# Optimization experiments

Measured on AMD Instinct MI355X. Metric: run time of the kernel, lower is better.

## Reference

```python
import jax, jax.numpy as jnp
import numpy as np

B, S, D, H = 8, 2048, 512, 8
NEG = -1e9


def setup_inputs() -> dict:
    key = jax.random.key(0)
    ks = jax.random.split(key, 12)
    inp = {
        "v": jax.random.normal(ks[0], (B, S, D), jnp.float32),
        "k": jax.random.normal(ks[1], (B, S, D), jnp.float32),
        "q": jax.random.normal(ks[2], (B, S, D), jnp.float32),
    }
    # pad_mask: 1.0 where key position is padding ([B,1,1,S]); random valid lengths
    lens = jax.random.randint(ks[3], (B,), S // 2, S + 1)
    inp["pad_mask"] = (jnp.arange(S)[None, :] >= lens[:, None]).astype(jnp.float32)[:, None, None, :]
    # head_mask: causal look-ahead mask, 1.0 above diagonal ([1,1,S,S])
    inp["head_mask"] = jnp.triu(jnp.ones((S, S), jnp.float32), k=1)[None, None]
    # Dense layer params (Keras Dense: y = x @ W + b)
    sc = 1.0 / np.sqrt(D)
    inp["Wq"] = jax.random.normal(ks[4], (D, D), jnp.float32) * sc
    inp["bq"] = jnp.zeros((D,), jnp.float32)
    inp["Wk"] = jax.random.normal(ks[5], (D, D), jnp.float32) * sc
    inp["bk"] = jnp.zeros((D,), jnp.float32)
    inp["Wv"] = jax.random.normal(ks[6], (D, D), jnp.float32) * sc
    inp["bv"] = jnp.zeros((D,), jnp.float32)
    inp["Wo"] = jax.random.normal(ks[7], (D, D), jnp.float32) * sc
    inp["bo"] = jnp.zeros((D,), jnp.float32)
    inp["num_heads"] = H
    return inp


def reference(v, k, q, pad_mask, head_mask, Wq, bq, Wk, bk, Wv, bv, Wo, bo, num_heads):
    b, s, d = q.shape
    depth = d // num_heads

    def split_heads(x):  # [b,s,d] -> [b,h,s,depth]
        return x.reshape(b, -1, num_heads, depth).transpose(0, 2, 1, 3)

    qh = split_heads(q @ Wq + bq)
    kh = split_heads(k @ Wk + bk)
    vh = split_heads(v @ Wv + bv)

    scale = 1.0 / jnp.sqrt(jnp.asarray(depth, qh.dtype))
    scores = jnp.einsum("bhqd,bhkd->bhqk", qh, kh) * scale
    scores = scores + pad_mask * NEG + head_mask * NEG
    attn = jax.nn.softmax(scores, axis=-1)
    ctx = jnp.einsum("bhqk,bhkd->bhqd", attn, vh)
    concat = ctx.transpose(0, 2, 1, 3).reshape(b, -1, d)
    return concat @ Wo + bo
```

## Files before the change

kernel.cpp:

```cpp
#include <hip/hip_runtime.h>

#define B_ 8
#define S_ 2048
#define D_ 512
#define H_ 8
#define HD_ 64

typedef __attribute__((ext_vector_type(8))) short short8;
typedef __attribute__((ext_vector_type(4))) short short4v;
typedef __attribute__((ext_vector_type(4))) float f32x4;
typedef __attribute__((ext_vector_type(16))) float f32x16;
typedef __attribute__((ext_vector_type(8))) __bf16 bf16x8;
typedef __attribute__((ext_vector_type(4))) unsigned uint4v;

__device__ __forceinline__ short f2bf(float f) {
    union { float f; unsigned u; } x; x.f = f;
    unsigned r = x.u + 0x7fffu + ((x.u >> 16) & 1u);
    return (short)(r >> 16);
}

__device__ __forceinline__ unsigned cvtpk(float a, float b) {
    unsigned r;
    asm("v_cvt_pk_bf16_f32 %0, %1, %2" : "=v"(r) : "v"(a), "v"(b));
    return r;
}

__device__ __forceinline__ f32x4 mfma16(short8 a, short8 b, f32x4 c) {
    return __builtin_amdgcn_mfma_f32_16x16x32_bf16(
        __builtin_bit_cast(bf16x8, a), __builtin_bit_cast(bf16x8, b), c, 0, 0, 0);
}

__device__ __forceinline__ f32x16 mfma32(short8 a, short8 b, f32x16 c) {
    return __builtin_amdgcn_mfma_f32_32x32x16_bf16(
        __builtin_bit_cast(bf16x8, a), __builtin_bit_cast(bf16x8, b), c, 0, 0, 0);
}

__device__ __forceinline__ f32x16 zero16() {
    f32x16 z;
    #pragma unroll
    for (int i = 0; i < 16; ++i) z[i] = 0.f;
    return z;
}

__global__ __launch_bounds__(256) void prep_wt(
    const float* __restrict__ W0, const float* __restrict__ W1,
    const float* __restrict__ W2, const float* __restrict__ W3,
    short* __restrict__ T0, short* __restrict__ T1,
    short* __restrict__ T2, short* __restrict__ T3)
{
    const float* W = (blockIdx.z == 0) ? W0 : (blockIdx.z == 1) ? W1 : (blockIdx.z == 2) ? W2 : W3;
    short* T = (blockIdx.z == 0) ? T0 : (blockIdx.z == 1) ? T1 : (blockIdx.z == 2) ? T2 : T3;
    __shared__ float t_s[64][65];
    const int tid = threadIdx.x;
    const int k0 = blockIdx.x * 64, n0 = blockIdx.y * 64;
    const int col = tid & 63, rg = tid >> 6;
    #pragma unroll
    for (int j = 0; j < 16; ++j) {
        const int row = rg * 16 + j;
        t_s[row][col] = W[(size_t)(k0 + row) * D_ + n0 + col];
    }
    __syncthreads();
    #pragma unroll
    for (int j = 0; j < 16; ++j) {
        const int nn = rg * 16 + j;
        T[(size_t)(n0 + nn) * D_ + k0 + col] = f2bf(t_s[col][nn]);
    }
}

__global__ __launch_bounds__(512) void qkv_gemm(
    const float* __restrict__ q_in, const float* __restrict__ k_in, const float* __restrict__ v_in,
    const short* __restrict__ wtq, const short* __restrict__ wtk, const short* __restrict__ wtv,
    const float* __restrict__ bq, const float* __restrict__ bk, const float* __restrict__ bv,
    short* __restrict__ qh, short* __restrict__ kh, short* __restrict__ vtb, float qscale)
{
    const int id = blockIdx.x;
    const int xcd = id & 7;
    const int slot = id >> 3;
    const int n0 = (slot & 3) * 128;
    const int pidx = xcd * 48 + (slot >> 2);
    const int z = pidx >> 7;
    const int m0 = (pidx & 127) * 128;

    const float* Ain = (z == 0) ? q_in : (z == 1) ? k_in : v_in;
    const short* Wt  = (z == 0) ? wtq  : (z == 1) ? wtk  : wtv;
    const float* bias = (z == 0) ? bq : (z == 1) ? bk : bv;
    short* Cout = (z == 0) ? qh : (z == 1) ? kh : vtb;
    const float osc = (z == 0) ? qscale : 1.0f;
    const int N = D_, K = D_;

    __shared__ __align__(16) short a_s[2][128 * 72];
    __shared__ __align__(16) short bt_s[2][128 * 72];

    const int tid = threadIdx.x;
    const int lane = tid & 63, wave = tid >> 6;
    const int wr = wave >> 2, wc = wave & 3;
    const int lr = lane & 15, lg = lane >> 4;

    const int srow = tid >> 3, sch = (tid & 7) * 8;

    f32x4 acc[4][2] = {};

    f32x4 fa[4];
    short8 bs[2];
    {
        const f32x4* ap0 = (const f32x4*)(Ain + (size_t)(m0 + srow) * K + sch);
        fa[0] = ap0[0]; fa[1] = ap0[1];
        const f32x4* ap1 = (const f32x4*)(Ain + (size_t)(m0 + srow + 64) * K + sch);
        fa[2] = ap1[0]; fa[3] = ap1[1];
        bs[0] = *(const short8*)(Wt + (size_t)(n0 + srow) * K + sch);
        bs[1] = *(const short8*)(Wt + (size_t)(n0 + srow + 64) * K + sch);
    }

    int cur = 0;
    for (int k0 = 0; k0 < K; k0 += 64) {
        {
            const uint4v u0 = { cvtpk(fa[0][0], fa[0][1]), cvtpk(fa[0][2], fa[0][3]),
                                cvtpk(fa[1][0], fa[1][1]), cvtpk(fa[1][2], fa[1][3]) };
            *(short8*)&a_s[cur][srow * 72 + sch] = __builtin_bit_cast(short8, u0);
            const uint4v u1 = { cvtpk(fa[2][0], fa[2][1]), cvtpk(fa[2][2], fa[2][3]),
                                cvtpk(fa[3][0], fa[3][1]), cvtpk(fa[3][2], fa[3][3]) };
            *(short8*)&a_s[cur][(srow + 64) * 72 + sch] = __builtin_bit_cast(short8, u1);
            *(short8*)&bt_s[cur][srow * 72 + sch] = bs[0];
            *(short8*)&bt_s[cur][(srow + 64) * 72 + sch] = bs[1];
        }
        __syncthreads();
        if (k0 + 64 < K) {
            const f32x4* ap0 = (const f32x4*)(Ain + (size_t)(m0 + srow) * K + k0 + 64 + sch);
            fa[0] = ap0[0]; fa[1] = ap0[1];
            const f32x4* ap1 = (const f32x4*)(Ain + (size_t)(m0 + srow + 64) * K + k0 + 64 + sch);
            fa[2] = ap1[0]; fa[3] = ap1[1];
            bs[0] = *(const short8*)(Wt + (size_t)(n0 + srow) * K + k0 + 64 + sch);
            bs[1] = *(const short8*)(Wt + (size_t)(n0 + srow + 64) * K + k0 + 64 + sch);
        }

        #pragma unroll
        for (int kc = 0; kc < 2; ++kc) {
            short8 af[4], bf[2];
            #pragma unroll
            for (int m = 0; m < 4; ++m)
                af[m] = *(const short8*)&a_s[cur][(wr * 64 + m * 16 + lr) * 72 + kc * 32 + lg * 8];
            #pragma unroll
            for (int n = 0; n < 2; ++n)
                bf[n] = *(const short8*)&bt_s[cur][(wc * 32 + n * 16 + lr) * 72 + kc * 32 + lg * 8];
            __builtin_amdgcn_s_setprio(1);
            #pragma unroll
            for (int m = 0; m < 4; ++m)
                #pragma unroll
                for (int n = 0; n < 2; ++n)
                    acc[m][n] = mfma16(af[m], bf[n], acc[m][n]);
            __builtin_amdgcn_s_setprio(0);
        }
        cur ^= 1;
    }

    float bvv[2];
    #pragma unroll
    for (int n = 0; n < 2; ++n) bvv[n] = bias[n0 + wc * 32 + n * 16 + lr];

    if (z == 2) {
        #pragma unroll
        for (int m = 0; m < 4; ++m) {
            const int row0 = m0 + wr * 64 + m * 16 + lg * 4;
            const int bb = row0 >> 11, s0 = row0 & (S_ - 1);
            #pragma unroll
            for (int n = 0; n < 2; ++n) {
                const int col = n0 + wc * 32 + n * 16 + lr;
                uint2 wv;
                wv.x = cvtpk(acc[m][n][0] + bvv[n], acc[m][n][1] + bvv[n]);
                wv.y = cvtpk(acc[m][n][2] + bvv[n], acc[m][n][3] + bvv[n]);
                *(uint2*)(Cout + ((size_t)col * B_ + bb) * S_ + s0) = wv;
            }
        }
    } else {
        #pragma unroll
        for (int m = 0; m < 4; ++m)
            #pragma unroll
            for (int i = 0; i < 4; ++i) {
                const size_t row = m0 + wr * 64 + m * 16 + lg * 4 + i;
                #pragma unroll
                for (int n = 0; n < 2; ++n) {
                    const int col = n0 + wc * 32 + n * 16 + lr;
                    Cout[row * N + col] = f2bf((acc[m][n][i] + bvv[n]) * osc);
                }
            }
    }
}

__global__ __launch_bounds__(512) void out_gemm(
    const short* __restrict__ Ain, const short* __restrict__ Wt,
    const float* __restrict__ bias, float* __restrict__ Cout)
{
    const int id = blockIdx.x;
    const int xcd = id & 7;
    const int slot = id >> 3;
    const int n0 = (slot & 3) * 128;
    const int m0 = (xcd * 16 + (slot >> 2)) * 128;
    const int N = D_, K = D_;

    __shared__ __align__(16) short a_s[2][128 * 72];
    __shared__ __align__(16) short bt_s[2][128 * 72];

    const int tid = threadIdx.x;
    const int lane = tid & 63, wave = tid >> 6;
    const int wr = wave >> 2, wc = wave & 3;
    const int lr = lane & 15, lg = lane >> 4;
    const int srow = tid >> 3, sch = (tid & 7) * 8;

    f32x4 acc[4][2] = {};

    short8 as[2], bs[2];
    {
        as[0] = *(const short8*)(Ain + (size_t)(m0 + srow) * K + sch);
        as[1] = *(const short8*)(Ain + (size_t)(m0 + srow + 64) * K + sch);
        bs[0] = *(const short8*)(Wt + (size_t)(n0 + srow) * K + sch);
        bs[1] = *(const short8*)(Wt + (size_t)(n0 + srow + 64) * K + sch);
    }

    int cur = 0;
    for (int k0 = 0; k0 < K; k0 += 64) {
        *(short8*)&a_s[cur][srow * 72 + sch] = as[0];
        *(short8*)&a_s[cur][(srow + 64) * 72 + sch] = as[1];
        *(short8*)&bt_s[cur][srow * 72 + sch] = bs[0];
        *(short8*)&bt_s[cur][(srow + 64) * 72 + sch] = bs[1];
        __syncthreads();
        if (k0 + 64 < K) {
            as[0] = *(const short8*)(Ain + (size_t)(m0 + srow) * K + k0 + 64 + sch);
            as[1] = *(const short8*)(Ain + (size_t)(m0 + srow + 64) * K + k0 + 64 + sch);
            bs[0] = *(const short8*)(Wt + (size_t)(n0 + srow) * K + k0 + 64 + sch);
            bs[1] = *(const short8*)(Wt + (size_t)(n0 + srow + 64) * K + k0 + 64 + sch);
        }

        #pragma unroll
        for (int kc = 0; kc < 2; ++kc) {
            short8 af[4], bf[2];
            #pragma unroll
            for (int m = 0; m < 4; ++m)
                af[m] = *(const short8*)&a_s[cur][(wr * 64 + m * 16 + lr) * 72 + kc * 32 + lg * 8];
            #pragma unroll
            for (int n = 0; n < 2; ++n)
                bf[n] = *(const short8*)&bt_s[cur][(wc * 32 + n * 16 + lr) * 72 + kc * 32 + lg * 8];
            __builtin_amdgcn_s_setprio(1);
            #pragma unroll
            for (int m = 0; m < 4; ++m)
                #pragma unroll
                for (int n = 0; n < 2; ++n)
                    acc[m][n] = mfma16(af[m], bf[n], acc[m][n]);
            __builtin_amdgcn_s_setprio(0);
        }
        cur ^= 1;
    }

    float bvv[2];
    #pragma unroll
    for (int n = 0; n < 2; ++n) bvv[n] = bias[n0 + wc * 32 + n * 16 + lr];
    #pragma unroll
    for (int m = 0; m < 4; ++m)
        #pragma unroll
        for (int i = 0; i < 4; ++i) {
            const size_t row = m0 + wr * 64 + m * 16 + lg * 4 + i;
            #pragma unroll
            for (int n = 0; n < 2; ++n)
                Cout[row * N + n0 + wc * 32 + n * 16 + lr] = acc[m][n][i] + bvv[n];
        }
}

__global__ __launch_bounds__(128, 3) void attn_k(
    const short* __restrict__ qh, const short* __restrict__ kh,
    const short* __restrict__ vt, const float* __restrict__ pad_mask,
    short* __restrict__ ctx)
{
    const int tid = threadIdx.x;
    const int lane = tid & 63, w = tid >> 6;
    const int l31 = lane & 31, hi = lane >> 5;
    const int id = blockIdx.x;
    const int h = id & 7;
    const int b = (id >> 3) & 7;
    const int pair = id >> 6;
    const int NT = S_ / 64;

    __shared__ __align__(16) short k_s[2][64 * 72];
    __shared__ __align__(16) short vt_s[2][64 * 68];
    __shared__ float red_s[2];

    const float* pb = pad_mask + (size_t)b * S_;
    {
        const f32x4* pv4 = (const f32x4*)pb;
        float psum = 0.f;
        #pragma unroll
        for (int j = 0; j < 4; ++j) {
            const f32x4 a = pv4[tid * 4 + j];
            psum += a[0] + a[1] + a[2] + a[3];
        }
        for (int off = 1; off < 64; off <<= 1) psum += __shfl_xor(psum, off);
        if (lane == 0) red_s[w] = psum;
    }
    __syncthreads();
    const int len = S_ - (int)(red_s[0] + red_s[1] + 0.5f);

    const int srow = tid >> 1, sc0 = (tid & 1) * 32;
    const short* kbase = kh + ((size_t)b * S_ + srow) * D_ + h * HD_ + sc0;
    const short* vbase = vt + ((size_t)(h * HD_ + srow) * B_ + b) * S_ + sc0;

    int cur = 0;
    for (int half = 0; half < 2; ++half) {
        const int qt = half ? (NT - 1 - pair) : pair;
        const int q0 = qt * 64;
        const int kt_end = min(qt, (len - 1) >> 6);

        const int qrow = q0 + 2 * l31 + w;
        const short* qptr = qh + ((size_t)b * S_ + qrow) * D_ + h * HD_ + hi * 8;
        short8 qf[4];
        #pragma unroll
        for (int dd = 0; dd < 4; ++dd) qf[dd] = *(const short8*)(qptr + dd * 16);

        f32x16 accA = zero16(), accB = zero16();
        float m_r = -1e30f, l_r = 0.f;
        const int kmax = min(qrow, len - 1);

        short8 kv[4], vv[4];
        #pragma unroll
        for (int p = 0; p < 4; ++p) {
            kv[p] = ((const short8*)kbase)[p];
            vv[p] = ((const short8*)vbase)[p];
        }

        for (int kt = 0; kt <= kt_end; ++kt) {
            #pragma unroll
            for (int p = 0; p < 4; ++p)
                *(short8*)&k_s[cur][srow * 72 + sc0 + p * 8] = kv[p];
            #pragma unroll
            for (int p = 0; p < 4; ++p) {
                *(short4v*)&vt_s[cur][srow * 68 + sc0 + p * 8]     = __builtin_shufflevector(vv[p], vv[p], 0, 1, 2, 3);
                *(short4v*)&vt_s[cur][srow * 68 + sc0 + p * 8 + 4] = __builtin_shufflevector(vv[p], vv[p], 4, 5, 6, 7);
            }
            __syncthreads();
            if (kt < kt_end) {
                const short* kp = kbase + (size_t)(kt + 1) * 64 * D_;
                const short* vp = vbase + (kt + 1) * 64;
                #pragma unroll
                for (int p = 0; p < 4; ++p) {
                    kv[p] = ((const short8*)kp)[p];
                    vv[p] = ((const short8*)vp)[p];
                }
            }

            f32x16 scA = zero16(), scB = zero16();
            __builtin_amdgcn_s_setprio(1);
            #pragma unroll
            for (int dd = 0; dd < 4; ++dd) {
                const short8 kfA = *(const short8*)&k_s[cur][l31 * 72 + dd * 16 + hi * 8];
                const short8 kfB = *(const short8*)&k_s[cur][(32 + l31) * 72 + dd * 16 + hi * 8];
                scA = mfma32(kfA, qf[dd], scA);
                scB = mfma32(kfB, qf[dd], scB);
            }
            __builtin_amdgcn_s_setprio(0);

            const bool needmask = (kt == qt) || (kt * 64 + 63 >= len);
            if (needmask) {
                #pragma unroll
                for (int reg = 0; reg < 16; ++reg) {
                    const int koff = kt * 64 + (reg & 3) + 8 * (reg >> 2) + 4 * hi;
                    if (koff > kmax)      scA[reg] = -1e30f;
                    if (koff + 32 > kmax) scB[reg] = -1e30f;
                }
            }

            float m8[8], m4[4];
            #pragma unroll
            for (int i = 0; i < 8; ++i) m8[i] = fmaxf(fmaxf(scA[i], scA[i + 8]), fmaxf(scB[i], scB[i + 8]));
            #pragma unroll
            for (int i = 0; i < 4; ++i) m4[i] = fmaxf(m8[i], m8[i + 4]);
            float mt = fmaxf(fmaxf(m4[0], m4[1]), fmaxf(m4[2], m4[3]));
            mt = fmaxf(mt, __shfl_xor(mt, 32));
            const bool nogrow = __all(mt <= m_r);
            const float mn = nogrow ? m_r : fmaxf(m_r, mt);

            #pragma unroll
            for (int i = 0; i < 16; ++i) {
                scA[i] = __builtin_amdgcn_exp2f(scA[i] - mn);
                scB[i] = __builtin_amdgcn_exp2f(scB[i] - mn);
            }
            float s8[8], s4[4];
            #pragma unroll
            for (int i = 0; i < 8; ++i) s8[i] = (scA[i] + scA[i + 8]) + (scB[i] + scB[i + 8]);
            #pragma unroll
            for (int i = 0; i < 4; ++i) s4[i] = s8[i] + s8[i + 4];
            float rs = (s4[0] + s4[1]) + (s4[2] + s4[3]);
            rs += __shfl_xor(rs, 32);

            if (nogrow) {
                l_r += rs;
            } else {
                const float fac = __builtin_amdgcn_exp2f(m_r - mn);
                l_r = l_r * fac + rs;
                m_r = mn;
                #pragma unroll
                for (int reg = 0; reg < 16; ++reg) { accA[reg] *= fac; accB[reg] *= fac; }
            }

            unsigned pw[4][4];
            #pragma unroll
            for (int kk = 0; kk < 4; ++kk) {
                const int g = kk & 1;
                unsigned w0, w1, w2, w3;
                if (kk < 2) {
                    w0 = cvtpk(scA[8 * g + 0], scA[8 * g + 1]);
                    w1 = cvtpk(scA[8 * g + 2], scA[8 * g + 3]);
                    w2 = cvtpk(scA[8 * g + 4], scA[8 * g + 5]);
                    w3 = cvtpk(scA[8 * g + 6], scA[8 * g + 7]);
                } else {
                    w0 = cvtpk(scB[8 * g + 0], scB[8 * g + 1]);
                    w1 = cvtpk(scB[8 * g + 2], scB[8 * g + 3]);
                    w2 = cvtpk(scB[8 * g + 4], scB[8 * g + 5]);
                    w3 = cvtpk(scB[8 * g + 6], scB[8 * g + 7]);
                }
                asm("v_permlane32_swap_b32 %0, %1" : "+v"(w0), "+v"(w2));
                asm("v_permlane32_swap_b32 %0, %1" : "+v"(w1), "+v"(w3));
                pw[kk][0] = w0; pw[kk][1] = w1; pw[kk][2] = w2; pw[kk][3] = w3;
            }

            __builtin_amdgcn_s_setprio(1);
            #pragma unroll
            for (int kk = 0; kk < 4; ++kk) {
                const uint4v u = { pw[kk][0], pw[kk][1], pw[kk][2], pw[kk][3] };
                const short8 pf = __builtin_bit_cast(short8, u);
                const short4v a0 = *(const short4v*)&vt_s[cur][l31 * 68 + kk * 16 + 8 * hi];
                const short4v a1 = *(const short4v*)&vt_s[cur][l31 * 68 + kk * 16 + 8 * hi + 4];
                const short8 afA = __builtin_shufflevector(a0, a1, 0, 1, 2, 3, 4, 5, 6, 7);
                accA = mfma32(afA, pf, accA);
                const short4v b0 = *(const short4v*)&vt_s[cur][(32 + l31) * 68 + kk * 16 + 8 * hi];
                const short4v b1 = *(const short4v*)&vt_s[cur][(32 + l31) * 68 + kk * 16 + 8 * hi + 4];
                const short8 afB = __builtin_shufflevector(b0, b1, 0, 1, 2, 3, 4, 5, 6, 7);
                accB = mfma32(afB, pf, accB);
            }
            __builtin_amdgcn_s_setprio(0);
            cur ^= 1;
        }

        const float li = __builtin_amdgcn_rcpf(l_r);
        short* cp = ctx + ((size_t)b * S_ + qrow) * D_ + h * HD_ + 4 * hi;
        #pragma unroll
        for (int g = 0; g < 4; ++g) {
            uint2 wa;
            wa.x = cvtpk(accA[4 * g + 0] * li, accA[4 * g + 1] * li);
            wa.y = cvtpk(accA[4 * g + 2] * li, accA[4 * g + 3] * li);
            *(uint2*)(cp + 8 * g) = wa;
            uint2 wb;
            wb.x = cvtpk(accB[4 * g + 0] * li, accB[4 * g + 1] * li);
            wb.y = cvtpk(accB[4 * g + 2] * li, accB[4 * g + 3] * li);
            *(uint2*)(cp + 32 + 8 * g) = wb;
        }
    }
}

extern "C" void kernel_launch(void* const* d_in, const int* in_sizes, int n_in,
                              void* d_out, int out_size, void* d_ws, size_t ws_size,
                              hipStream_t stream)
{
    const float* v_in = (const float*)d_in[0];
    const float* k_in = (const float*)d_in[1];
    const float* q_in = (const float*)d_in[2];
    const float* pad  = (const float*)d_in[3];
    const float* Wq = (const float*)d_in[5];  const float* bq = (const float*)d_in[6];
    const float* Wk = (const float*)d_in[7];  const float* bk = (const float*)d_in[8];
    const float* Wv = (const float*)d_in[9];  const float* bv = (const float*)d_in[10];
    const float* Wo = (const float*)d_in[11]; const float* bo = (const float*)d_in[12];

    const size_t elems = (size_t)B_ * S_ * D_;
    const size_t welems = (size_t)D_ * D_;
    short* qh  = (short*)d_ws;
    short* kh  = qh + elems;
    short* vtb = kh + elems;
    short* ctx = vtb + elems;
    short* wtq = ctx + elems;
    short* wtk = wtq + welems;
    short* wtv = wtk + welems;
    short* wto = wtv + welems;

    prep_wt<<<dim3(D_ / 64, D_ / 64, 4), dim3(256), 0, stream>>>(Wq, Wk, Wv, Wo, wtq, wtk, wtv, wto);

    const float qscale = 0.125f * 1.4426950408889634f;
    qkv_gemm<<<dim3(1536), dim3(512), 0, stream>>>(
        q_in, k_in, v_in, wtq, wtk, wtv, bq, bk, bv, qh, kh, vtb, qscale);

    attn_k<<<dim3(1024), dim3(128), 0, stream>>>(qh, kh, vtb, pad, ctx);

    out_gemm<<<dim3(512), dim3(512), 0, stream>>>(ctx, wto, bo, (float*)d_out);
}
```

Measured before the change: 135.6 us.

## Split attention KV loop across two waves with 32-row query tiles

The attention kernel now processes 32-query tiles (grid doubled to 2048 blocks). The two waves in each block take alternating 32-key tiles independently, each with its own LDS buffer, so the per-iteration block barrier goes away. At the end the two partial softmax states and accumulators are merged through shared memory. Occupancy hint raised from 3 to 4 blocks. This trades halved MFMA work per wave step and an extra cross-wave merge for finer load balance and no intra-loop syncs.

```diff
diff --git a/kernel.cpp b/kernel.cpp
--- a/kernel.cpp
+++ b/kernel.cpp
@@ -95,7 +95,6 @@
     const int lane = tid & 63, wave = tid >> 6;
     const int wr = wave >> 2, wc = wave & 3;
     const int lr = lane & 15, lg = lane >> 4;
-
     const int srow = tid >> 3, sch = (tid & 7) * 8;
 
     f32x4 acc[4][2] = {};
@@ -264,7 +263,7 @@
         }
 }
 
-__global__ __launch_bounds__(128, 3) void attn_k(
+__global__ __launch_bounds__(128, 4) void attn_k(
     const short* __restrict__ qh, const short* __restrict__ kh,
     const short* __restrict__ vt, const float* __restrict__ pad_mask,
     short* __restrict__ ctx)
@@ -275,11 +274,10 @@
     const int id = blockIdx.x;
     const int h = id & 7;
     const int b = (id >> 3) & 7;
-    const int pair = id >> 6;
-    const int NT = S_ / 64;
-
-    __shared__ __align__(16) short k_s[2][64 * 72];
-    __shared__ __align__(16) short vt_s[2][64 * 68];
+    const int p = id >> 6;
+
+    __shared__ __align__(16) short k_s[2][32 * 68];
+    __shared__ __align__(16) short vs_s[2][64 * 36];
     __shared__ float red_s[2];
 
     const float* pb = pad_mask + (size_t)b * S_;
@@ -297,17 +295,21 @@
     __syncthreads();
     const int len = S_ - (int)(red_s[0] + red_s[1] + 0.5f);
 
-    const int srow = tid >> 1, sc0 = (tid & 1) * 32;
-    const short* kbase = kh + ((size_t)b * S_ + srow) * D_ + h * HD_ + sc0;
-    const short* vbase = vt + ((size_t)(h * HD_ + srow) * B_ + b) * S_ + sc0;
-
-    int cur = 0;
+    const int ksr = lane >> 1, ksc = (lane & 1) * 32;
+    const short* kbase = kh + ((size_t)b * S_ + ksr) * D_ + h * HD_ + ksc;
+    const short* vbase = vt + ((size_t)(h * HD_ + lane) * B_ + b) * S_;
+
+    float* accx = (float*)&k_s[0][0];
+    float* mx = (float*)&vs_s[0][0];
+    float* lx = mx + 128;
+
     for (int half = 0; half < 2; ++half) {
-        const int qt = half ? (NT - 1 - pair) : pair;
-        const int q0 = qt * 64;
-        const int kt_end = min(qt, (len - 1) >> 6);
-
-        const int qrow = q0 + 2 * l31 + w;
+        const int qt = half ? (63 - p) : p;
+        const int q0 = qt * 32;
+        const int kt_end = min(qt, (len - 1) >> 5);
+        const int qrow = q0 + l31;
+        const int kmax = min(qrow, len - 1);
+
         const short* qptr = qh + ((size_t)b * S_ + qrow) * D_ + h * HD_ + hi * 8;
         short8 qf[4];
         #pragma unroll
@@ -315,59 +317,52 @@
 
         f32x16 accA = zero16(), accB = zero16();
         float m_r = -1e30f, l_r = 0.f;
-        const int kmax = min(qrow, len - 1);
-
+
+        int kt = w;
         short8 kv[4], vv[4];
-        #pragma unroll
-        for (int p = 0; p < 4; ++p) {
-            kv[p] = ((const short8*)kbase)[p];
-            vv[p] = ((const short8*)vbase)[p];
-        }
-
-        for (int kt = 0; kt <= kt_end; ++kt) {
-            #pragma unroll
-            for (int p = 0; p < 4; ++p)
-                *(short8*)&k_s[cur][srow * 72 + sc0 + p * 8] = kv[p];
-            #pragma unroll
-            for (int p = 0; p < 4; ++p) {
-                *(short4v*)&vt_s[cur][srow * 68 + sc0 + p * 8]     = __builtin_shufflevector(vv[p], vv[p], 0, 1, 2, 3);
-                *(short4v*)&vt_s[cur][srow * 68 + sc0 + p * 8 + 4] = __builtin_shufflevector(vv[p], vv[p], 4, 5, 6, 7);
-            }
-            __syncthreads();
-            if (kt < kt_end) {
-                const short* kp = kbase + (size_t)(kt + 1) * 64 * D_;
-                const short* vp = vbase + (kt + 1) * 64;
-                #pragma unroll
-                for (int p = 0; p < 4; ++p) {
-                    kv[p] = ((const short8*)kp)[p];
-                    vv[p] = ((const short8*)vp)[p];
+        if (kt <= kt_end) {
+            #pragma unroll
+            for (int pp = 0; pp < 4; ++pp) {
+                kv[pp] = *(const short8*)(kbase + (size_t)kt * 32 * D_ + pp * 8);
+                vv[pp] = *(const short8*)(vbase + kt * 32 + pp * 8);
+            }
+        }
+
+        for (; kt <= kt_end; kt += 2) {
+            #pragma unroll
+            for (int pp = 0; pp < 4; ++pp)
+                *(short8*)&k_s[w][ksr * 68 + ksc + pp * 8] = kv[pp];
+            #pragma unroll
+            for (int pp = 0; pp < 4; ++pp)
+                *(short8*)&vs_s[w][lane * 36 + pp * 8] = vv[pp];
+            if (kt + 2 <= kt_end) {
+                #pragma unroll
+                for (int pp = 0; pp < 4; ++pp) {
+                    kv[pp] = *(const short8*)(kbase + (size_t)(kt + 2) * 32 * D_ + pp * 8);
+                    vv[pp] = *(const short8*)(vbase + (kt + 2) * 32 + pp * 8);
                 }
             }
 
-            f32x16 scA = zero16(), scB = zero16();
+            f32x16 sc = zero16();
             __builtin_amdgcn_s_setprio(1);
             #pragma unroll
             for (int dd = 0; dd < 4; ++dd) {
-                const short8 kfA = *(const short8*)&k_s[cur][l31 * 72 + dd * 16 + hi * 8];
-                const short8 kfB = *(const short8*)&k_s[cur][(32 + l31) * 72 + dd * 16 + hi * 8];
-                scA = mfma32(kfA, qf[dd], scA);
-                scB = mfma32(kfB, qf[dd], scB);
+                const short8 kf = *(const short8*)&k_s[w][l31 * 68 + dd * 16 + hi * 8];
+                sc = mfma32(kf, qf[dd], sc);
             }
             __builtin_amdgcn_s_setprio(0);
 
-            const bool needmask = (kt == qt) || (kt * 64 + 63 >= len);
-            if (needmask) {
+            if (kt == qt || kt * 32 + 31 >= len) {
                 #pragma unroll
                 for (int reg = 0; reg < 16; ++reg) {
-                    const int koff = kt * 64 + (reg & 3) + 8 * (reg >> 2) + 4 * hi;
-                    if (koff > kmax)      scA[reg] = -1e30f;
-                    if (koff + 32 > kmax) scB[reg] = -1e30f;
+                    const int koff = kt * 32 + (reg & 3) + 8 * (reg >> 2) + 4 * hi;
+                    if (koff > kmax) sc[reg] = -1e30f;
                 }
             }
 
             float m8[8], m4[4];
             #pragma unroll
-            for (int i = 0; i < 8; ++i) m8[i] = fmaxf(fmaxf(scA[i], scA[i + 8]), fmaxf(scB[i], scB[i + 8]));
+            for (int i = 0; i < 8; ++i) m8[i] = fmaxf(sc[i], sc[i + 8]);
             #pragma unroll
             for (int i = 0; i < 4; ++i) m4[i] = fmaxf(m8[i], m8[i + 4]);
             float mt = fmaxf(fmaxf(m4[0], m4[1]), fmaxf(m4[2], m4[3]));
@@ -376,13 +371,10 @@
             const float mn = nogrow ? m_r : fmaxf(m_r, mt);
 
             #pragma unroll
-            for (int i = 0; i < 16; ++i) {
-                scA[i] = __builtin_amdgcn_exp2f(scA[i] - mn);
-                scB[i] = __builtin_amdgcn_exp2f(scB[i] - mn);
-            }
+            for (int i = 0; i < 16; ++i) sc[i] = __builtin_amdgcn_exp2f(sc[i] - mn);
             float s8[8], s4[4];
             #pragma unroll
-            for (int i = 0; i < 8; ++i) s8[i] = (scA[i] + scA[i + 8]) + (scB[i] + scB[i + 8]);
+            for (int i = 0; i < 8; ++i) s8[i] = sc[i] + sc[i + 8];
             #pragma unroll
             for (int i = 0; i < 4; ++i) s4[i] = s8[i] + s8[i + 4];
             float rs = (s4[0] + s4[1]) + (s4[2] + s4[3]);
@@ -398,22 +390,13 @@
                 for (int reg = 0; reg < 16; ++reg) { accA[reg] *= fac; accB[reg] *= fac; }
             }
 
-            unsigned pw[4][4];
-            #pragma unroll
-            for (int kk = 0; kk < 4; ++kk) {
-                const int g = kk & 1;
-                unsigned w0, w1, w2, w3;
-                if (kk < 2) {
-                    w0 = cvtpk(scA[8 * g + 0], scA[8 * g + 1]);
-                    w1 = cvtpk(scA[8 * g + 2], scA[8 * g + 3]);
-                    w2 = cvtpk(scA[8 * g + 4], scA[8 * g + 5]);
-                    w3 = cvtpk(scA[8 * g + 6], scA[8 * g + 7]);
-                } else {
-                    w0 = cvtpk(scB[8 * g + 0], scB[8 * g + 1]);
-                    w1 = cvtpk(scB[8 * g + 2], scB[8 * g + 3]);
-                    w2 = cvtpk(scB[8 * g + 4], scB[8 * g + 5]);
-                    w3 = cvtpk(scB[8 * g + 6], scB[8 * g + 7]);
-                }
+            unsigned pw[2][4];
+            #pragma unroll
+            for (int kk = 0; kk < 2; ++kk) {
+                unsigned w0 = cvtpk(sc[8 * kk + 0], sc[8 * kk + 1]);
+                unsigned w1 = cvtpk(sc[8 * kk + 2], sc[8 * kk + 3]);
+                unsigned w2 = cvtpk(sc[8 * kk + 4], sc[8 * kk + 5]);
+                unsigned w3 = cvtpk(sc[8 * kk + 6], sc[8 * kk + 7]);
                 asm("v_permlane32_swap_b32 %0, %1" : "+v"(w0), "+v"(w2));
                 asm("v_permlane32_swap_b32 %0, %1" : "+v"(w1), "+v"(w3));
                 pw[kk][0] = w0; pw[kk][1] = w1; pw[kk][2] = w2; pw[kk][3] = w3;
@@ -421,35 +404,58 @@
 
             __builtin_amdgcn_s_setprio(1);
             #pragma unroll
-            for (int kk = 0; kk < 4; ++kk) {
+            for (int kk = 0; kk < 2; ++kk) {
                 const uint4v u = { pw[kk][0], pw[kk][1], pw[kk][2], pw[kk][3] };
                 const short8 pf = __builtin_bit_cast(short8, u);
-                const short4v a0 = *(const short4v*)&vt_s[cur][l31 * 68 + kk * 16 + 8 * hi];
-                const short4v a1 = *(const short4v*)&vt_s[cur][l31 * 68 + kk * 16 + 8 * hi + 4];
+                const short4v a0 = *(const short4v*)&vs_s[w][l31 * 36 + kk * 16 + 8 * hi];
+                const short4v a1 = *(const short4v*)&vs_s[w][l31 * 36 + kk * 16 + 8 * hi + 4];
                 const short8 afA = __builtin_shufflevector(a0, a1, 0, 1, 2, 3, 4, 5, 6, 7);
                 accA = mfma32(afA, pf, accA);
-                const short4v b0 = *(const short4v*)&vt_s[cur][(32 + l31) * 68 + kk * 16 + 8 * hi];
-                const short4v b1 = *(const short4v*)&vt_s[cur][(32 + l31) * 68 + kk * 16 + 8 * hi + 4];
+                const short4v b0 = *(const short4v*)&vs_s[w][(32 + l31) * 36 + kk * 16 + 8 * hi];
+                const short4v b1 = *(const short4v*)&vs_s[w][(32 + l31) * 36 + kk * 16 + 8 * hi + 4];
                 const short8 afB = __builtin_shufflevector(b0, b1, 0, 1, 2, 3, 4, 5, 6, 7);
                 accB = mfma32(afB, pf, accB);
             }
             __builtin_amdgcn_s_setprio(0);
-            cur ^= 1;
-        }
-
-        const float li = __builtin_amdgcn_rcpf(l_r);
-        short* cp = ctx + ((size_t)b * S_ + qrow) * D_ + h * HD_ + 4 * hi;
-        #pragma unroll
-        for (int g = 0; g < 4; ++g) {
-            uint2 wa;
-            wa.x = cvtpk(accA[4 * g + 0] * li, accA[4 * g + 1] * li);
-            wa.y = cvtpk(accA[4 * g + 2] * li, accA[4 * g + 3] * li);
-            *(uint2*)(cp + 8 * g) = wa;
-            uint2 wb;
-            wb.x = cvtpk(accB[4 * g + 0] * li, accB[4 * g + 1] * li);
-            wb.y = cvtpk(accB[4 * g + 2] * li, accB[4 * g + 3] * li);
-            *(uint2*)(cp + 32 + 8 * g) = wb;
-        }
+        }
+
+        __syncthreads();
+        mx[w * 64 + lane] = m_r;
+        lx[w * 64 + lane] = l_r;
+        __syncthreads();
+        const float mo = mx[(w ^ 1) * 64 + lane];
+        const float lo = lx[(w ^ 1) * 64 + lane];
+        const float mj = fmaxf(m_r, mo);
+        const float facS = __builtin_amdgcn_exp2f(m_r - mj);
+        const float facO = __builtin_amdgcn_exp2f(mo - mj);
+        const float l_tot = l_r * facS + lo * facO;
+        if (w == 1) {
+            #pragma unroll
+            for (int i = 0; i < 16; ++i) accx[i * 64 + lane] = accA[i] * facS;
+            #pragma unroll
+            for (int i = 0; i < 16; ++i) accx[(16 + i) * 64 + lane] = accB[i] * facS;
+        }
+        __syncthreads();
+        if (w == 0) {
+            const float li = __builtin_amdgcn_rcpf(l_tot);
+            short* cp = ctx + ((size_t)b * S_ + qrow) * D_ + h * HD_ + 4 * hi;
+            #pragma unroll
+            for (int g = 0; g < 4; ++g) {
+                float o0 = (accA[4 * g + 0] * facS + accx[(4 * g + 0) * 64 + lane]) * li;
+                float o1 = (accA[4 * g + 1] * facS + accx[(4 * g + 1) * 64 + lane]) * li;
+                float o2 = (accA[4 * g + 2] * facS + accx[(4 * g + 2) * 64 + lane]) * li;
+                float o3 = (accA[4 * g + 3] * facS + accx[(4 * g + 3) * 64 + lane]) * li;
+                uint2 wa; wa.x = cvtpk(o0, o1); wa.y = cvtpk(o2, o3);
+                *(uint2*)(cp + 8 * g) = wa;
+                float p0 = (accB[4 * g + 0] * facS + accx[(16 + 4 * g + 0) * 64 + lane]) * li;
+                float p1 = (accB[4 * g + 1] * facS + accx[(16 + 4 * g + 1) * 64 + lane]) * li;
+                float p2 = (accB[4 * g + 2] * facS + accx[(16 + 4 * g + 2) * 64 + lane]) * li;
+                float p3 = (accB[4 * g + 3] * facS + accx[(16 + 4 * g + 3) * 64 + lane]) * li;
+                uint2 wb; wb.x = cvtpk(p0, p1); wb.y = cvtpk(p2, p3);
+                *(uint2*)(cp + 32 + 8 * g) = wb;
+            }
+        }
+        __syncthreads();
     }
 }
 
@@ -483,7 +489,7 @@
     qkv_gemm<<<dim3(1536), dim3(512), 0, stream>>>(
         q_in, k_in, v_in, wtq, wtk, wtv, bq, bk, bv, qh, kh, vtb, qscale);
 
-    attn_k<<<dim3(1024), dim3(128), 0, stream>>>(qh, kh, vtb, pad, ctx);
+    attn_k<<<dim3(2048), dim3(128), 0, stream>>>(qh, kh, vtb, pad, ctx);
 
     out_gemm<<<dim3(512), dim3(512), 0, stream>>>(ctx, wto, bo, (float*)d_out);
 }
```

New measurement: 195.3 us. +44.1%, slower.

## Make attention waves independent with per-wave K/V tiles and no block barriers

Applied to the files above, without the earlier changes.

Restructures the attention kernel so each of the two waves in a block owns a 32-row query tile (paired causally as p and 63-p) and stages its own 64-key K/V tile in a private LDS slot. This removes all __syncthreads from the key loop and the shared pad-mask reduction, and the grid is doubled to 2048 blocks. Each wave now loads a full K/V tile by itself, so global and LDS traffic per query row doubles, the single LDS buffer per wave loses double buffering, and launch bounds drop to 2 blocks per SIMD.

```diff
diff --git a/kernel.cpp b/kernel.cpp
--- a/kernel.cpp
+++ b/kernel.cpp
@@ -95,7 +95,6 @@
     const int lane = tid & 63, wave = tid >> 6;
     const int wr = wave >> 2, wc = wave & 3;
     const int lr = lane & 15, lg = lane >> 4;
-
     const int srow = tid >> 3, sch = (tid & 7) * 8;
 
     f32x4 acc[4][2] = {};
@@ -264,7 +263,7 @@
         }
 }
 
-__global__ __launch_bounds__(128, 3) void attn_k(
+__global__ __launch_bounds__(128, 2) void attn_k(
     const short* __restrict__ qh, const short* __restrict__ kh,
     const short* __restrict__ vt, const float* __restrict__ pad_mask,
     short* __restrict__ ctx)
@@ -275,181 +274,170 @@
     const int id = blockIdx.x;
     const int h = id & 7;
     const int b = (id >> 3) & 7;
-    const int pair = id >> 6;
-    const int NT = S_ / 64;
+    const int p = id >> 6;
 
     __shared__ __align__(16) short k_s[2][64 * 72];
     __shared__ __align__(16) short vt_s[2][64 * 68];
-    __shared__ float red_s[2];
-
-    const float* pb = pad_mask + (size_t)b * S_;
+
+    float psum = 0.f;
     {
-        const f32x4* pv4 = (const f32x4*)pb;
-        float psum = 0.f;
-        #pragma unroll
-        for (int j = 0; j < 4; ++j) {
-            const f32x4 a = pv4[tid * 4 + j];
-            psum += a[0] + a[1] + a[2] + a[3];
-        }
+        const f32x4* pv4 = (const f32x4*)(pad_mask + (size_t)b * S_);
+        #pragma unroll
+        for (int j = 0; j < 8; ++j) {
+            const f32x4 a = pv4[lane * 8 + j];
+            psum += (a[0] + a[1]) + (a[2] + a[3]);
+        }
+        #pragma unroll
         for (int off = 1; off < 64; off <<= 1) psum += __shfl_xor(psum, off);
-        if (lane == 0) red_s[w] = psum;
-    }
-    __syncthreads();
-    const int len = S_ - (int)(red_s[0] + red_s[1] + 0.5f);
-
-    const int srow = tid >> 1, sc0 = (tid & 1) * 32;
-    const short* kbase = kh + ((size_t)b * S_ + srow) * D_ + h * HD_ + sc0;
-    const short* vbase = vt + ((size_t)(h * HD_ + srow) * B_ + b) * S_ + sc0;
-
-    int cur = 0;
-    for (int half = 0; half < 2; ++half) {
-        const int qt = half ? (NT - 1 - pair) : pair;
-        const int q0 = qt * 64;
-        const int kt_end = min(qt, (len - 1) >> 6);
-
-        const int qrow = q0 + 2 * l31 + w;
-        const short* qptr = qh + ((size_t)b * S_ + qrow) * D_ + h * HD_ + hi * 8;
-        short8 qf[4];
-        #pragma unroll
-        for (int dd = 0; dd < 4; ++dd) qf[dd] = *(const short8*)(qptr + dd * 16);
-
-        f32x16 accA = zero16(), accB = zero16();
-        float m_r = -1e30f, l_r = 0.f;
-        const int kmax = min(qrow, len - 1);
-
-        short8 kv[4], vv[4];
-        #pragma unroll
-        for (int p = 0; p < 4; ++p) {
-            kv[p] = ((const short8*)kbase)[p];
-            vv[p] = ((const short8*)vbase)[p];
-        }
-
-        for (int kt = 0; kt <= kt_end; ++kt) {
-            #pragma unroll
-            for (int p = 0; p < 4; ++p)
-                *(short8*)&k_s[cur][srow * 72 + sc0 + p * 8] = kv[p];
-            #pragma unroll
-            for (int p = 0; p < 4; ++p) {
-                *(short4v*)&vt_s[cur][srow * 68 + sc0 + p * 8]     = __builtin_shufflevector(vv[p], vv[p], 0, 1, 2, 3);
-                *(short4v*)&vt_s[cur][srow * 68 + sc0 + p * 8 + 4] = __builtin_shufflevector(vv[p], vv[p], 4, 5, 6, 7);
+    }
+    const int len = S_ - (int)(psum + 0.5f);
+    const int lenT = (len - 1) >> 6;
+
+    const int qt = w ? (63 - p) : p;
+    const int q0 = qt * 32;
+    const int diag = qt >> 1;
+    const int kt_end = min(diag, lenT);
+    const int qrow = q0 + l31;
+    const int kmax = min(qrow, len - 1);
+
+    const short* qptr = qh + ((size_t)b * S_ + qrow) * D_ + h * HD_ + hi * 8;
+    short8 qf[4];
+    #pragma unroll
+    for (int dd = 0; dd < 4; ++dd) qf[dd] = *(const short8*)(qptr + dd * 16);
+
+    f32x16 accA = zero16(), accB = zero16();
+    float m_r = -1e30f, l_r = 0.f;
+
+    const short* kbase = kh + ((size_t)b * S_ + lane) * D_ + h * HD_;
+    const short* vbase = vt + ((size_t)(h * HD_ + lane) * B_ + b) * S_;
+
+    short8 kv[8], vv[8];
+    #pragma unroll
+    for (int pp = 0; pp < 8; ++pp) {
+        kv[pp] = *(const short8*)(kbase + pp * 8);
+        vv[pp] = *(const short8*)(vbase + pp * 8);
+    }
+
+    for (int kt = 0; kt <= kt_end; ++kt) {
+        #pragma unroll
+        for (int pp = 0; pp < 8; ++pp)
+            *(short8*)&k_s[w][lane * 72 + pp * 8] = kv[pp];
+        #pragma unroll
+        for (int pp = 0; pp < 8; ++pp)
+            *(short8*)&vt_s[w][lane * 68 + pp * 8] = vv[pp];
+        if (kt < kt_end) {
+            const short* kp = kbase + (size_t)(kt + 1) * 64 * D_;
+            const short* vp = vbase + (kt + 1) * 64;
+            #pragma unroll
+            for (int pp = 0; pp < 8; ++pp) {
+                kv[pp] = *(const short8*)(kp + pp * 8);
+                vv[pp] = *(const short8*)(vp + pp * 8);
             }
-            __syncthreads();
-            if (kt < kt_end) {
-                const short* kp = kbase + (size_t)(kt + 1) * 64 * D_;
-                const short* vp = vbase + (kt + 1) * 64;
-                #pragma unroll
-                for (int p = 0; p < 4; ++p) {
-                    kv[p] = ((const short8*)kp)[p];
-                    vv[p] = ((const short8*)vp)[p];
-                }
+        }
+
+        f32x16 scA = zero16(), scB = zero16();
+        __builtin_amdgcn_s_setprio(1);
+        #pragma unroll
+        for (int dd = 0; dd < 4; ++dd) {
+            const short8 kfA = *(const short8*)&k_s[w][l31 * 72 + dd * 16 + hi * 8];
+            const short8 kfB = *(const short8*)&k_s[w][(32 + l31) * 72 + dd * 16 + hi * 8];
+            scA = mfma32(kfA, qf[dd], scA);
+            scB = mfma32(kfB, qf[dd], scB);
+        }
+        __builtin_amdgcn_s_setprio(0);
+
+        if (kt == diag || kt * 64 + 63 >= len) {
+            #pragma unroll
+            for (int reg = 0; reg < 16; ++reg) {
+                const int koff = kt * 64 + (reg & 3) + 8 * (reg >> 2) + 4 * hi;
+                if (koff > kmax)      scA[reg] = -1e30f;
+                if (koff + 32 > kmax) scB[reg] = -1e30f;
             }
-
-            f32x16 scA = zero16(), scB = zero16();
-            __builtin_amdgcn_s_setprio(1);
-            #pragma unroll
-            for (int dd = 0; dd < 4; ++dd) {
-                const short8 kfA = *(const short8*)&k_s[cur][l31 * 72 + dd * 16 + hi * 8];
-                const short8 kfB = *(const short8*)&k_s[cur][(32 + l31) * 72 + dd * 16 + hi * 8];
-                scA = mfma32(kfA, qf[dd], scA);
-                scB = mfma32(kfB, qf[dd], scB);
+        }
+
+        float m8[8], m4[4];
+        #pragma unroll
+        for (int i = 0; i < 8; ++i) m8[i] = fmaxf(fmaxf(scA[i], scA[i + 8]), fmaxf(scB[i], scB[i + 8]));
+        #pragma unroll
+        for (int i = 0; i < 4; ++i) m4[i] = fmaxf(m8[i], m8[i + 4]);
+        float mt = fmaxf(fmaxf(m4[0], m4[1]), fmaxf(m4[2], m4[3]));
+        mt = fmaxf(mt, __shfl_xor(mt, 32));
+        const bool nogrow = __all(mt <= m_r);
+        const float mn = nogrow ? m_r : fmaxf(m_r, mt);
+
+        #pragma unroll
+        for (int i = 0; i < 16; ++i) {
+            scA[i] = __builtin_amdgcn_exp2f(scA[i] - mn);
+            scB[i] = __builtin_amdgcn_exp2f(scB[i] - mn);
+        }
+        float s8[8], s4[4];
+        #pragma unroll
+        for (int i = 0; i < 8; ++i) s8[i] = (scA[i] + scA[i + 8]) + (scB[i] + scB[i + 8]);
+        #pragma unroll
+        for (int i = 0; i < 4; ++i) s4[i] = s8[i] + s8[i + 4];
+        float rs = (s4[0] + s4[1]) + (s4[2] + s4[3]);
+        rs += __shfl_xor(rs, 32);
+
+        if (nogrow) {
+            l_r += rs;
+        } else {
+            const float fac = __builtin_amdgcn_exp2f(m_r - mn);
+            l_r = l_r * fac + rs;
+            m_r = mn;
+            #pragma unroll
+            for (int reg = 0; reg < 16; ++reg) { accA[reg] *= fac; accB[reg] *= fac; }
+        }
+
+        unsigned pw[4][4];
+        #pragma unroll
+        for (int kk = 0; kk < 4; ++kk) {
+            const int g = kk & 1;
+            unsigned w0, w1, w2, w3;
+            if (kk < 2) {
+                w0 = cvtpk(scA[8 * g + 0], scA[8 * g + 1]);
+                w1 = cvtpk(scA[8 * g + 2], scA[8 * g + 3]);
+                w2 = cvtpk(scA[8 * g + 4], scA[8 * g + 5]);
+                w3 = cvtpk(scA[8 * g + 6], scA[8 * g + 7]);
+            } else {
+                w0 = cvtpk(scB[8 * g + 0], scB[8 * g + 1]);
+                w1 = cvtpk(scB[8 * g + 2], scB[8 * g + 3]);
+                w2 = cvtpk(scB[8 * g + 4], scB[8 * g + 5]);
+                w3 = cvtpk(scB[8 * g + 6], scB[8 * g + 7]);
             }
-            __builtin_amdgcn_s_setprio(0);
-
-            const bool needmask = (kt == qt) || (kt * 64 + 63 >= len);
-            if (needmask) {
-                #pragma unroll
-                for (int reg = 0; reg < 16; ++reg) {
-                    const int koff = kt * 64 + (reg & 3) + 8 * (reg >> 2) + 4 * hi;
-                    if (koff > kmax)      scA[reg] = -1e30f;
-                    if (koff + 32 > kmax) scB[reg] = -1e30f;
-                }
-            }
-
-            float m8[8], m4[4];
-            #pragma unroll
-            for (int i = 0; i < 8; ++i) m8[i] = fmaxf(fmaxf(scA[i], scA[i + 8]), fmaxf(scB[i], scB[i + 8]));
-            #pragma unroll
-            for (int i = 0; i < 4; ++i) m4[i] = fmaxf(m8[i], m8[i + 4]);
-            float mt = fmaxf(fmaxf(m4[0], m4[1]), fmaxf(m4[2], m4[3]));
-            mt = fmaxf(mt, __shfl_xor(mt, 32));
-            const bool nogrow = __all(mt <= m_r);
-            const float mn = nogrow ? m_r : fmaxf(m_r, mt);
-
-            #pragma unroll
-            for (int i = 0; i < 16; ++i) {
-                scA[i] = __builtin_amdgcn_exp2f(scA[i] - mn);
-                scB[i] = __builtin_amdgcn_exp2f(scB[i] - mn);
-            }
-            float s8[8], s4[4];
-            #pragma unroll
-            for (int i = 0; i < 8; ++i) s8[i] = (scA[i] + scA[i + 8]) + (scB[i] + scB[i + 8]);
-            #pragma unroll
-            for (int i = 0; i < 4; ++i) s4[i] = s8[i] + s8[i + 4];
-            float rs = (s4[0] + s4[1]) + (s4[2] + s4[3]);
-            rs += __shfl_xor(rs, 32);
-
-            if (nogrow) {
-                l_r += rs;
-            } else {
-                const float fac = __builtin_amdgcn_exp2f(m_r - mn);
-                l_r = l_r * fac + rs;
-                m_r = mn;
-                #pragma unroll
-                for (int reg = 0; reg < 16; ++reg) { accA[reg] *= fac; accB[reg] *= fac; }
-            }
-
-            unsigned pw[4][4];
-            #pragma unroll
-            for (int kk = 0; kk < 4; ++kk) {
-                const int g = kk & 1;
-                unsigned w0, w1, w2, w3;
-                if (kk < 2) {
-                    w0 = cvtpk(scA[8 * g + 0], scA[8 * g + 1]);
-                    w1 = cvtpk(scA[8 * g + 2], scA[8 * g + 3]);
-                    w2 = cvtpk(scA[8 * g + 4], scA[8 * g + 5]);
-                    w3 = cvtpk(scA[8 * g + 6], scA[8 * g + 7]);
-                } else {
-                    w0 = cvtpk(scB[8 * g + 0], scB[8 * g + 1]);
-                    w1 = cvtpk(scB[8 * g + 2], scB[8 * g + 3]);
-                    w2 = cvtpk(scB[8 * g + 4], scB[8 * g + 5]);
-                    w3 = cvtpk(scB[8 * g + 6], scB[8 * g + 7]);
-                }
-                asm("v_permlane32_swap_b32 %0, %1" : "+v"(w0), "+v"(w2));
-                asm("v_permlane32_swap_b32 %0, %1" : "+v"(w1), "+v"(w3));
-                pw[kk][0] = w0; pw[kk][1] = w1; pw[kk][2] = w2; pw[kk][3] = w3;
-            }
-
-            __builtin_amdgcn_s_setprio(1);
-            #pragma unroll
-            for (int kk = 0; kk < 4; ++kk) {
-                const uint4v u = { pw[kk][0], pw[kk][1], pw[kk][2], pw[kk][3] };
-                const short8 pf = __builtin_bit_cast(short8, u);
-                const short4v a0 = *(const short4v*)&vt_s[cur][l31 * 68 + kk * 16 + 8 * hi];
-                const short4v a1 = *(const short4v*)&vt_s[cur][l31 * 68 + kk * 16 + 8 * hi + 4];
-                const short8 afA = __builtin_shufflevector(a0, a1, 0, 1, 2, 3, 4, 5, 6, 7);
-                accA = mfma32(afA, pf, accA);
-                const short4v b0 = *(const short4v*)&vt_s[cur][(32 + l31) * 68 + kk * 16 + 8 * hi];
-                const short4v b1 = *(const short4v*)&vt_s[cur][(32 + l31) * 68 + kk * 16 + 8 * hi + 4];
-                const short8 afB = __builtin_shufflevector(b0, b1, 0, 1, 2, 3, 4, 5, 6, 7);
-                accB = mfma32(afB, pf, accB);
-            }
-            __builtin_amdgcn_s_setprio(0);
-            cur ^= 1;
-        }
-
-        const float li = __builtin_amdgcn_rcpf(l_r);
-        short* cp = ctx + ((size_t)b * S_ + qrow) * D_ + h * HD_ + 4 * hi;
-        #pragma unroll
-        for (int g = 0; g < 4; ++g) {
-            uint2 wa;
-            wa.x = cvtpk(accA[4 * g + 0] * li, accA[4 * g + 1] * li);
-            wa.y = cvtpk(accA[4 * g + 2] * li, accA[4 * g + 3] * li);
-            *(uint2*)(cp + 8 * g) = wa;
-            uint2 wb;
-            wb.x = cvtpk(accB[4 * g + 0] * li, accB[4 * g + 1] * li);
-            wb.y = cvtpk(accB[4 * g + 2] * li, accB[4 * g + 3] * li);
-            *(uint2*)(cp + 32 + 8 * g) = wb;
-        }
+            asm("v_permlane32_swap_b32 %0, %1" : "+v"(w0), "+v"(w2));
+            asm("v_permlane32_swap_b32 %0, %1" : "+v"(w1), "+v"(w3));
+            pw[kk][0] = w0; pw[kk][1] = w1; pw[kk][2] = w2; pw[kk][3] = w3;
+        }
+
+        __builtin_amdgcn_s_setprio(1);
+        #pragma unroll
+        for (int kk = 0; kk < 4; ++kk) {
+            const uint4v u = { pw[kk][0], pw[kk][1], pw[kk][2], pw[kk][3] };
+            const short8 pf = __builtin_bit_cast(short8, u);
+            const short4v a0 = *(const short4v*)&vt_s[w][l31 * 68 + kk * 16 + 8 * hi];
+            const short4v a1 = *(const short4v*)&vt_s[w][l31 * 68 + kk * 16 + 8 * hi + 4];
+            const short8 afA = __builtin_shufflevector(a0, a1, 0, 1, 2, 3, 4, 5, 6, 7);
+            accA = mfma32(afA, pf, accA);
+            const short4v b0 = *(const short4v*)&vt_s[w][(32 + l31) * 68 + kk * 16 + 8 * hi];
+            const short4v b1 = *(const short4v*)&vt_s[w][(32 + l31) * 68 + kk * 16 + 8 * hi + 4];
+            const short8 afB = __builtin_shufflevector(b0, b1, 0, 1, 2, 3, 4, 5, 6, 7);
+            accB = mfma32(afB, pf, accB);
+        }
+        __builtin_amdgcn_s_setprio(0);
+    }
+
+    const float li = __builtin_amdgcn_rcpf(l_r);
+    short* cp = ctx + ((size_t)b * S_ + qrow) * D_ + h * HD_ + 4 * hi;
+    #pragma unroll
+    for (int g = 0; g < 4; ++g) {
+        uint2 wa;
+        wa.x = cvtpk(accA[4 * g + 0] * li, accA[4 * g + 1] * li);
+        wa.y = cvtpk(accA[4 * g + 2] * li, accA[4 * g + 3] * li);
+        *(uint2*)(cp + 8 * g) = wa;
+        uint2 wb;
+        wb.x = cvtpk(accB[4 * g + 0] * li, accB[4 * g + 1] * li);
+        wb.y = cvtpk(accB[4 * g + 2] * li, accB[4 * g + 3] * li);
+        *(uint2*)(cp + 32 + 8 * g) = wb;
     }
 }
 
@@ -483,7 +471,7 @@
     qkv_gemm<<<dim3(1536), dim3(512), 0, stream>>>(
         q_in, k_in, v_in, wtq, wtk, wtv, bq, bk, bv, qh, kh, vtb, qscale);
 
-    attn_k<<<dim3(1024), dim3(128), 0, stream>>>(qh, kh, vtb, pad, ctx);
+    attn_k<<<dim3(2048), dim3(128), 0, stream>>>(qh, kh, vtb, pad, ctx);
 
     out_gemm<<<dim3(512), dim3(512), 0, stream>>>(ctx, wto, bo, (float*)d_out);
 }
```

Result: slower. 196.6 us (+45.0%).
